# Kernel optimization log

Measured on AMD Instinct MI355X. Metric: run time of the kernel, lower is better.

## Reference

```python
import jax, jax.numpy as jnp
import numpy as np

NEG = -1e30   # safe -inf surrogate
EPS = 1e-7    # keras.backend.epsilon() used by ctc_batch_cost


def setup_inputs() -> dict:
    key = jax.random.key(0)
    k1, k2 = jax.random.split(key)
    B, T, C, L = 512, 512, 256, 64
    u = jax.random.uniform(k1, (B, T, C), dtype=jnp.float32, minval=1e-3, maxval=1.0)
    y_pred = u / jnp.sum(u, axis=-1, keepdims=True)  # softmax-like probabilities
    y_true = jax.random.randint(k2, (B, L), 0, C - 1)  # labels in [0, C-2]; blank = C-1
    return {"y_true": y_true, "y_pred": y_pred}


def ctc_loss(y_true, y_pred):
    # Faithful to K.ctc_batch_cost with label_length = L, input_length = T for all samples.
    B, T, C = y_pred.shape
    L = y_true.shape[1]
    S = 2 * L + 1            # extended label length (blanks interleaved)
    blank = C - 1            # TF CTC convention: blank is last class
    labels = y_true.astype(jnp.int32)

    # extended labels: [blank, l1, blank, l2, ..., lL, blank]
    ext = jnp.full((B, S), blank, dtype=jnp.int32).at[:, 1::2].set(labels)
    prev2 = jnp.concatenate([jnp.full((B, 2), blank, jnp.int32), ext[:, :-2]], axis=1)
    # transition s-2 -> s allowed only for non-blank states with ext[s] != ext[s-2]
    skip = (ext != blank) & (ext != prev2)

    logp = jnp.log(y_pred + EPS)                                   # [B,T,C]
    idx = jnp.broadcast_to(ext[:, None, :], (B, T, S))
    lp_ext = jnp.take_along_axis(logp, idx, axis=2)                # [B,T,S]

    # alpha at t=0: only states 0 (blank) and 1 (first label) reachable
    alpha0 = jnp.full((B, S), NEG, dtype=logp.dtype)
    alpha0 = alpha0.at[:, 0].set(lp_ext[:, 0, 0]).at[:, 1].set(lp_ext[:, 0, 1])

    def step(alpha, lp_t):
        a1 = jnp.concatenate([jnp.full((B, 1), NEG, alpha.dtype), alpha[:, :-1]], axis=1)
        a2 = jnp.concatenate([jnp.full((B, 2), NEG, alpha.dtype), alpha[:, :-2]], axis=1)
        m = jnp.logaddexp(jnp.logaddexp(alpha, a1), jnp.where(skip, a2, NEG))
        return m + lp_t, None

    lp_seq = jnp.transpose(lp_ext, (1, 0, 2))[1:]                  # [T-1,B,S]
    alphaT, _ = jax.lax.scan(step, alpha0, lp_seq)

    # total log-likelihood ends in last blank or last label
    loss = -jnp.logaddexp(alphaT[:, S - 1], alphaT[:, S - 2])      # [B]
    return loss[:, None]                                           # [B,1] like ctc_batch_cost


def reference(y_true, y_pred):
    return ctc_loss(y_true, y_pred)
```

## Files before the change

kernel.cpp:

```cpp
#include <hip/hip_runtime.h>


#define NEGF (-1e30f)
#define EPSF (1e-7f)

constexpr int T_   = 512;
constexpr int C_   = 256;
constexpr int L_   = 64;
constexpr int TCH  = 16;
constexpr int NCH  = T_ / TCH;
constexpr int NROW = 64;
constexpr int PD   = 8;

__device__ __forceinline__ float lae2(float a, float b) {
    float m = fmaxf(a, b);
    float d = fminf(a, b) - m;
    return m + __logf(1.0f + __expf(d));
}

__device__ __forceinline__ float wave_shr1(float x) {
    int r = __builtin_amdgcn_update_dpp(0, __float_as_int(x),
                                        0x138 ,
                                        0xF, 0xF, true );
    return __int_as_float(r);
}

typedef const __attribute__((address_space(1))) void GV;
typedef __attribute__((address_space(3))) void LV;

__global__ __launch_bounds__(64, 1)
void ctc_kernel(const int* __restrict__ y_true,
                const float* __restrict__ y_pred,
                float* __restrict__ out) {
    __shared__ float tile[NROW * C_];

    const int b     = blockIdx.x;
    const int lane  = threadIdx.x;
    const int blank = C_ - 1;

    const int* lab  = y_true + b * L_;
    const int e1    = lab[lane];
    const int eprev = (lane == 0) ? blank : lab[lane - 1];
    const bool skip1 = (e1 != blank) && (e1 != eprev);

    const float* __restrict__ row = y_pred + (size_t)b * T_ * C_;

    auto issue_chunk = [&](int c) {
        const float* src = row + (size_t)c * TCH * C_ + lane * 4;
        float* dst = &tile[((c * TCH) & (NROW - 1)) * C_];
#pragma unroll
        for (int r = 0; r < TCH; ++r) {
            __builtin_amdgcn_global_load_lds((GV*)(src + r * C_),
                                             (LV*)(dst + r * C_),
                                             16, 0, 0);
        }
    };

    issue_chunk(0); issue_chunk(1); issue_chunk(2); issue_chunk(3);
    __builtin_amdgcn_s_waitcnt(0x8F70);

    float plp0[PD], plp1[PD];
#pragma unroll
    for (int j = 0; j < PD; ++j) {
        float p0 = tile[j * C_ + blank];
        float p1 = tile[j * C_ + e1];
        plp0[j] = __logf(p0 + EPSF);
        plp1[j] = __logf(p1 + EPSF);
    }

    float a0 = NEGF, a1 = NEGF, a2 = NEGF;

    for (int c = 0; c < NCH; ++c) {
        if (c > 0) {
            const int cn = c + 3;
            if (cn < NCH) {
                issue_chunk(cn);
                __builtin_amdgcn_s_waitcnt(0x8F70);
            } else if (c + 2 < NCH) {
                __builtin_amdgcn_s_waitcnt(0x4F70);
            } else {
                __builtin_amdgcn_s_waitcnt(0x0F70);
            }
        }
#pragma unroll
        for (int j = 0; j < TCH; ++j) {
            const int t = c * TCH + j;
            const float lp0 = plp0[j & (PD - 1)];
            const float lp1 = plp1[j & (PD - 1)];

            int tn = t + PD; if (tn > T_ - 1) tn = T_ - 1;
            const int rbase = (tn & (NROW - 1)) * C_;
            const float q0 = tile[rbase + blank];
            const float q1 = tile[rbase + e1];
            plp0[j & (PD - 1)] = __logf(q0 + EPSF);
            plp1[j & (PD - 1)] = __logf(q1 + EPSF);

            if (c == 0 && j == 0) {
                a0 = (lane == 0) ? lp0 : NEGF;
                a1 = (lane == 0) ? lp1 : NEGF;
                a2 = NEGF;
            } else {
                float pa1 = wave_shr1(a1);
                if (lane == 0) pa1 = NEGF;

                const float na0 = lae2(a0, pa1) + lp0;

                const float c3 = skip1 ? pa1 : NEGF;
                const float m  = fmaxf(fmaxf(a1, a0), c3);
                const float s  = __expf(a1 - m) + __expf(a0 - m) + __expf(c3 - m);
                const float na1 = m + __logf(s) + lp1;

                const float na2 = lae2(a2, a1) + lp0;

                a0 = na0; a1 = na1; a2 = na2;
            }
        }
    }

    if (lane == 63) {
        out[b] = -lae2(a1, a2);
    }
}

extern "C" void kernel_launch(void* const* d_in, const int* in_sizes, int n_in,
                              void* d_out, int out_size, void* d_ws, size_t ws_size,
                              hipStream_t stream) {
    const int*   y_true = (const int*)d_in[0];
    const float* y_pred = (const float*)d_in[1];
    float*       out    = (float*)d_out;

    const int B = in_sizes[0] / L_;
    ctc_kernel<<<dim3(B), dim3(64), 0, stream>>>(y_true, y_pred, out);
}
```

Baseline: 402.1 us.

## Specialize warps: three producer waves stage and log-transform, one wave runs recurrence

Changes each block from a single wave to four. Three producer waves stream y_pred chunks into double-buffered LDS and precompute the log-probabilities for the blank and each lane's label. The consumer wave only reads the precomputed values and runs the alpha recurrence, with a block barrier per chunk. The goal is to move the load and log work off the serial critical path. The cost is a __syncthreads every 16 timesteps and a higher per-block thread count, which may limit how many blocks are resident.

```diff
diff --git a/kernel.cpp b/kernel.cpp
--- a/kernel.cpp
+++ b/kernel.cpp
@@ -4,13 +4,11 @@
 #define NEGF (-1e30f)
 #define EPSF (1e-7f)
 
-constexpr int T_   = 512;
-constexpr int C_   = 256;
-constexpr int L_   = 64;
-constexpr int TCH  = 16;
-constexpr int NCH  = T_ / TCH;
-constexpr int NROW = 64;
-constexpr int PD   = 8;
+constexpr int T_  = 512;
+constexpr int C_  = 256;
+constexpr int L_  = 64;
+constexpr int TCH = 16;
+constexpr int NCH = T_ / TCH;
 
 __device__ __forceinline__ float lae2(float a, float b) {
     float m = fmaxf(a, b);
@@ -28,73 +26,78 @@
 typedef const __attribute__((address_space(1))) void GV;
 typedef __attribute__((address_space(3))) void LV;
 
-__global__ __launch_bounds__(64, 1)
+__global__ __launch_bounds__(256, 1)
 void ctc_kernel(const int* __restrict__ y_true,
                 const float* __restrict__ y_pred,
                 float* __restrict__ out) {
-    __shared__ float tile[NROW * C_];
+    __shared__ float rawb[2][TCH * C_];
+    __shared__ float lpLs[2][TCH][64];
+    __shared__ float lpBs[2][TCH];
 
     const int b     = blockIdx.x;
-    const int lane  = threadIdx.x;
+    const int tid   = threadIdx.x;
+    const int lane  = tid & 63;
+    const int wid   = tid >> 6;
     const int blank = C_ - 1;
-
-    const int* lab  = y_true + b * L_;
-    const int e1    = lab[lane];
-    const int eprev = (lane == 0) ? blank : lab[lane - 1];
-    const bool skip1 = (e1 != blank) && (e1 != eprev);
 
     const float* __restrict__ row = y_pred + (size_t)b * T_ * C_;
 
-    auto issue_chunk = [&](int c) {
-        const float* src = row + (size_t)c * TCH * C_ + lane * 4;
-        float* dst = &tile[((c * TCH) & (NROW - 1)) * C_];
-#pragma unroll
-        for (int r = 0; r < TCH; ++r) {
-            __builtin_amdgcn_global_load_lds((GV*)(src + r * C_),
-                                             (LV*)(dst + r * C_),
-                                             16, 0, 0);
+    if (wid != 0) {
+        const int e1 = y_true[b * L_ + lane];
+
+        auto stage = [&](int c, int buf) {
+            const float* s = row + (size_t)c * TCH * C_ + lane * 4;
+            for (int r = wid - 1; r < TCH; r += 3) {
+                __builtin_amdgcn_global_load_lds((GV*)(s + r * C_),
+                                                 (LV*)(&rawb[buf][r * C_]),
+                                                 16, 0, 0);
+            }
+        };
+        auto produce = [&](int buf) {
+            for (int r = wid - 1; r < TCH; r += 3) {
+                float pe = rawb[buf][r * C_ + e1];
+                float pb = rawb[buf][r * C_ + blank];
+                lpLs[buf][r][lane] = __logf(pe + EPSF);
+                if (lane == 0) lpBs[buf][r] = __logf(pb + EPSF);
+            }
+        };
+
+        stage(0, 0);
+        stage(1, 1);
+        __builtin_amdgcn_s_waitcnt(0x0F70);
+        produce(0);
+        __syncthreads();
+
+        for (int c = 0; c < NCH; ++c) {
+            if (c + 2 < NCH) stage(c + 2, c & 1);
+            if (c + 1 < NCH) produce((c + 1) & 1);
+            __syncthreads();
         }
-    };
+        return;
+    }
 
-    issue_chunk(0); issue_chunk(1); issue_chunk(2); issue_chunk(3);
-    __builtin_amdgcn_s_waitcnt(0x8F70);
-
-    float plp0[PD], plp1[PD];
-#pragma unroll
-    for (int j = 0; j < PD; ++j) {
-        float p0 = tile[j * C_ + blank];
-        float p1 = tile[j * C_ + e1];
-        plp0[j] = __logf(p0 + EPSF);
-        plp1[j] = __logf(p1 + EPSF);
-    }
+    const int e1    = y_true[b * L_ + lane];
+    const int eprev = (lane == 0) ? blank : y_true[b * L_ + lane - 1];
+    const bool skip1 = (e1 != blank) && (e1 != eprev);
 
     float a0 = NEGF, a1 = NEGF, a2 = NEGF;
 
+    __syncthreads();
+
     for (int c = 0; c < NCH; ++c) {
-        if (c > 0) {
-            const int cn = c + 3;
-            if (cn < NCH) {
-                issue_chunk(cn);
-                __builtin_amdgcn_s_waitcnt(0x8F70);
-            } else if (c + 2 < NCH) {
-                __builtin_amdgcn_s_waitcnt(0x4F70);
-            } else {
-                __builtin_amdgcn_s_waitcnt(0x0F70);
-            }
-        }
+        const int cb = c & 1;
+
+        float l0[TCH], l1[TCH];
 #pragma unroll
         for (int j = 0; j < TCH; ++j) {
-            const int t = c * TCH + j;
-            const float lp0 = plp0[j & (PD - 1)];
-            const float lp1 = plp1[j & (PD - 1)];
+            l1[j] = lpLs[cb][j][lane];
+            l0[j] = lpBs[cb][j];
+        }
 
-            int tn = t + PD; if (tn > T_ - 1) tn = T_ - 1;
-            const int rbase = (tn & (NROW - 1)) * C_;
-            const float q0 = tile[rbase + blank];
-            const float q1 = tile[rbase + e1];
-            plp0[j & (PD - 1)] = __logf(q0 + EPSF);
-            plp1[j & (PD - 1)] = __logf(q1 + EPSF);
-
+#pragma unroll
+        for (int j = 0; j < TCH; ++j) {
+            const float lp0 = l0[j];
+            const float lp1 = l1[j];
             if (c == 0 && j == 0) {
                 a0 = (lane == 0) ? lp0 : NEGF;
                 a1 = (lane == 0) ? lp1 : NEGF;
@@ -115,6 +118,7 @@
                 a0 = na0; a1 = na1; a2 = na2;
             }
         }
+        __syncthreads();
     }
 
     if (lane == 63) {
@@ -130,5 +134,5 @@
     float*       out    = (float*)d_out;
 
     const int B = in_sizes[0] / L_;
-    ctc_kernel<<<dim3(B), dim3(64), 0, stream>>>(y_true, y_pred, out);
+    ctc_kernel<<<dim3(B), dim3(256), 0, stream>>>(y_true, y_pred, out);
 }
```

New measurement: 366.8 us. 1.1x faster.
